# Kernel optimization log

Hardware: AMD Instinct MI355X
Metric: run time of the kernel (lower is better)

Reference implementation:

```python
import jax, jax.numpy as jnp
import numpy as np
from jax.ops import segment_sum

N = 100000
E = 1600000
IN_DIM = 128
HID_DIM = 128
OUT_DIM = 64
BN_EPS = 1e-5


def setup_inputs() -> dict:
    key = jax.random.key(0)
    ks = jax.random.split(key, 8)
    h = jax.random.normal(ks[0], (N, IN_DIM), dtype=jnp.float32)
    src = jax.random.randint(ks[1], (E,), 0, N, dtype=jnp.int32)
    dst = jax.random.randint(ks[2], (E,), 0, N, dtype=jnp.int32)
    # GraphConv weights (glorot-ish scale)
    W1 = jax.random.normal(ks[3], (IN_DIM, HID_DIM), dtype=jnp.float32) / np.sqrt(IN_DIM)
    b1 = jnp.zeros((HID_DIM,), dtype=jnp.float32)
    W2 = jax.random.normal(ks[4], (HID_DIM, OUT_DIM), dtype=jnp.float32) / np.sqrt(HID_DIM)
    b2 = jnp.zeros((OUT_DIM,), dtype=jnp.float32)
    gamma = jnp.ones((HID_DIM,), dtype=jnp.float32)
    beta = jnp.zeros((HID_DIM,), dtype=jnp.float32)
    return {"h": h, "W1": W1, "b1": b1, "W2": W2, "b2": b2,
            "gamma": gamma, "beta": beta, "src": src, "dst": dst}


def _graph_conv(h, W, b, src, dst):
    # DGL GraphConv, norm='both':
    # out = D_dst^{-1/2} * A^T (D_src^{-1/2} * h) W + b, degrees clamped to >=1
    ones = jnp.ones((E,), dtype=h.dtype)
    deg_out = jnp.clip(segment_sum(ones, src, num_segments=N), 1.0)  # out-degree of src
    deg_in = jnp.clip(segment_sum(ones, dst, num_segments=N), 1.0)   # in-degree of dst
    h = h * jax.lax.rsqrt(deg_out)[:, None]
    # apply weight before aggregation when it reduces/keeps dim (DGL optimization)
    if W.shape[0] >= W.shape[1]:
        h = h @ W
        agg = segment_sum(h[src], dst, num_segments=N)  # [N, out_feat]
    else:
        agg = segment_sum(h[src], dst, num_segments=N) @ W
    return agg * jax.lax.rsqrt(deg_in)[:, None] + b


def reference(h, W1, b1, W2, b2, gamma, beta, src, dst):
    h = _graph_conv(h, W1, b1, src, dst)           # [N, HID_DIM]
    # BatchNorm1d, training mode: batch stats over node axis, biased variance
    mean = jnp.mean(h, axis=0)
    var = jnp.mean((h - mean) ** 2, axis=0)
    h = (h - mean) * jax.lax.rsqrt(var + BN_EPS) * gamma + beta
    h = jax.nn.relu(h)
    # dropout p=0.0 -> identity
    h = _graph_conv(h, W2, b2, src, dst)           # [N, OUT_DIM]
    return h
```

## Files before the change

kernel.cpp:

```cpp
#include <hip/hip_runtime.h>

#define NN 100000
#define NE 1600000
#define NB 391
#define CAP 5120
#define EPB 8192
#define NG1 6250
#define NBN 64
#define BN_EPS 1e-5f

typedef _Float16 f16;
typedef _Float16 f16x4 __attribute__((ext_vector_type(4)));
typedef _Float16 f16x8 __attribute__((ext_vector_type(8)));
typedef float f32x4v __attribute__((ext_vector_type(4)));

__global__ __launch_bounds__(256) void kInit(const float* __restrict__ W1,
                                             const float* __restrict__ W2,
                                             f16* __restrict__ W1t,
                                             f16* __restrict__ W2t,
                                             int* __restrict__ curD,
                                             int* __restrict__ curS,
                                             float* __restrict__ stats,
                                             int* __restrict__ done) {
    int idx = blockIdx.x * 256 + threadIdx.x;
    if (idx < NB) { curD[idx] = idx * CAP; curS[idx] = idx * CAP; }
    if (idx < 512) stats[idx] = 0.f;
    if (idx == 512) done[0] = 0;
    if (idx < 16384) {
        int n = idx >> 7, k = idx & 127;
        W1t[idx] = (f16)W1[k * 128 + n];
    } else if (idx < 24576) {
        int j = idx - 16384;
        int n = j >> 7, k = j & 127;
        W2t[j] = (f16)W2[k * 64 + n];
    }
}

__global__ __launch_bounds__(512) void kC(const int* __restrict__ src,
                                          const int* __restrict__ dst,
                                          int* __restrict__ curD,
                                          int* __restrict__ curS,
                                          unsigned* __restrict__ pairs,
                                          unsigned char* __restrict__ srcBuck) {
    __shared__ int sA[EPB], dA[EPB];
    __shared__ int hD[NB], hS[NB], bD_[NB], bS_[NB];
    int t = threadIdx.x;
    for (int i = t; i < NB; i += 512) { hD[i] = 0; hS[i] = 0; }
    __syncthreads();
    int e0 = blockIdx.x * EPB;
    int ne = min(EPB, NE - e0);
    for (int i = t; i < ne; i += 512) {
        int s = src[e0 + i], d = dst[e0 + i];
        sA[i] = s; dA[i] = d;
        atomicAdd(&hD[d >> 8], 1);
        atomicAdd(&hS[s >> 8], 1);
    }
    __syncthreads();
    for (int i = t; i < NB; i += 512) {
        bD_[i] = hD[i] ? atomicAdd(&curD[i], hD[i]) : 0;
        bS_[i] = hS[i] ? atomicAdd(&curS[i], hS[i]) : 0;
        hD[i] = 0; hS[i] = 0;
    }
    __syncthreads();
    for (int i = t; i < ne; i += 512) {
        int s = sA[i], d = dA[i];
        int db = d >> 8, sb = s >> 8;
        int rD = atomicAdd(&hD[db], 1);
        int posD = bD_[db] + rD;
        int limD = (db + 1) * CAP - 1;
        if (posD > limD) posD = limD;
        pairs[posD] = ((unsigned)s << 8) | (unsigned)(d & 255);
        int rS = atomicAdd(&hS[sb], 1);
        int posS = bS_[sb] + rS;
        int limS = (sb + 1) * CAP - 1;
        if (posS > limS) posS = limS;
        srcBuck[posS] = (unsigned char)(s & 255);
    }
}

__global__ __launch_bounds__(256) void kDE(const unsigned* __restrict__ pairs,
                                           const unsigned char* __restrict__ srcBuck,
                                           const int* __restrict__ curD,
                                           const int* __restrict__ curS,
                                           int* __restrict__ rowS,
                                           int* __restrict__ rowE,
                                           int* __restrict__ col,
                                           int* __restrict__ degO) {
    __shared__ unsigned bufA[CAP];
    __shared__ int cnt[256], csc[256];
    int t = threadIdx.x;
    if (blockIdx.x < NB) {
        int b = blockIdx.x;
        int p0 = b * CAP;
        int n = min(curD[b] - p0, CAP);
        cnt[t] = 0;
        __syncthreads();
        for (int i = t; i < n; i += 256) {
            unsigned v = pairs[p0 + i];
            bufA[i] = v;
            atomicAdd(&cnt[v & 255u], 1);
        }
        __syncthreads();
        int vN = cnt[t];
        csc[t] = vN;
        __syncthreads();
        for (int off = 1; off < 256; off <<= 1) {
            int x = (t >= off) ? csc[t - off] : 0;
            __syncthreads();
            csc[t] += x;
            __syncthreads();
        }
        int nodeStart = csc[t] - vN;
        int node = b * 256 + t;
        if (node < NN) { rowS[node] = p0 + nodeStart; rowE[node] = p0 + nodeStart + vN; }
        cnt[t] = nodeStart;
        __syncthreads();
        for (int i = t; i < n; i += 256) {
            unsigned v = bufA[i];
            int r = atomicAdd(&cnt[v & 255u], 1);
            col[p0 + r] = (int)(v >> 8);
        }
    } else {
        int b = blockIdx.x - NB;
        cnt[t] = 0;
        __syncthreads();
        int p0 = b * CAP;
        int p1 = min(curS[b], p0 + CAP);
        for (int p = p0 + t; p < p1; p += 256)
            atomicAdd(&cnt[srcBuck[p]], 1);
        __syncthreads();
        int node = b * 256 + t;
        if (node < NN) degO[node] = cnt[t];
    }
}

__global__ __launch_bounds__(256) void k_gemm1(const float* __restrict__ h,
                                               const f16* __restrict__ W1t,
                                               const int* __restrict__ degO,
                                               f16* __restrict__ x1h) {
    __shared__ f16 Ah[128 * 128];
    __shared__ f16 Bt[128 * 128];
    __shared__ float rsA[128];
    int tid = threadIdx.x;
    int row0 = blockIdx.x * 128;
    if (tid < 128) {
        int r = row0 + tid;
        float d = (r < NN) ? (float)degO[r] : 1.f;
        rsA[tid] = rsqrtf(fmaxf(d, 1.f));
    }
#pragma unroll
    for (int p = 0; p < 8; ++p) {
        int fi = p * 256 + tid;
        int r = fi >> 4, c = fi & 15;
        uint4 v = *(const uint4*)&W1t[fi * 8];
        *(uint4*)&Bt[r * 128 + ((c ^ (r & 7)) * 8)] = v;
    }
    __syncthreads();
#pragma unroll
    for (int p = 0; p < 16; ++p) {
        int fi = p * 256 + tid;
        int r = fi >> 5, c4 = fi & 31;
        int grow = row0 + r;
        float4 av = float4{0.f, 0.f, 0.f, 0.f};
        if (grow < NN) av = *(const float4*)&h[(size_t)grow * 128 + c4 * 4];
        float rs = rsA[r];
        f16x4 t;
        t[0] = (f16)(av.x * rs); t[1] = (f16)(av.y * rs);
        t[2] = (f16)(av.z * rs); t[3] = (f16)(av.w * rs);
        int c8 = c4 >> 1, off = (c4 & 1) * 4;
        *(f16x4*)&Ah[r * 128 + ((c8 ^ (r & 7)) * 8) + off] = t;
    }
    __syncthreads();
    int l = tid & 63, w = tid >> 6;
    int lr = l & 15, g = l >> 4;
    int m0 = w * 32;
    f16x8 a[2][4];
#pragma unroll
    for (int m = 0; m < 2; ++m)
#pragma unroll
        for (int kk = 0; kk < 4; ++kk) {
            int row = m0 + m * 16 + lr;
            a[m][kk] = *(f16x8*)&Ah[row * 128 + (((kk * 4 + g) ^ (row & 7)) * 8)];
        }
    f32x4v acc[2][8];
#pragma unroll
    for (int m = 0; m < 2; ++m)
#pragma unroll
        for (int n = 0; n < 8; ++n) acc[m][n] = f32x4v{0.f, 0.f, 0.f, 0.f};
#pragma unroll
    for (int n = 0; n < 8; ++n) {
        int colr = n * 16 + lr;
        f16x8 b[4];
#pragma unroll
        for (int kk = 0; kk < 4; ++kk)
            b[kk] = *(f16x8*)&Bt[colr * 128 + (((kk * 4 + g) ^ (colr & 7)) * 8)];
#pragma unroll
        for (int m = 0; m < 2; ++m)
#pragma unroll
            for (int kk = 0; kk < 4; ++kk)
                acc[m][n] = __builtin_amdgcn_mfma_f32_16x16x32_f16(a[m][kk], b[kk], acc[m][n], 0, 0, 0);
    }
    __syncthreads();
#pragma unroll
    for (int m = 0; m < 2; ++m)
#pragma unroll
        for (int n = 0; n < 8; ++n)
#pragma unroll
            for (int q = 0; q < 4; ++q) {
                int row = m0 + m * 16 + g * 4 + q;
                Ah[row * 128 + n * 16 + lr] = (f16)acc[m][n][q];
            }
    __syncthreads();
#pragma unroll
    for (int p = 0; p < 8; ++p) {
        int idx = p * 64 + l;
        int r = idx >> 4, c = idx & 15;
        int row = m0 + r, grow = row0 + row;
        uint4 v = *(uint4*)&Ah[row * 128 + c * 8];
        if (grow < NN) *(uint4*)&x1h[(size_t)grow * 128 + c * 8] = v;
    }
}

__global__ __launch_bounds__(256) void k_gather1(const f16* __restrict__ x1h,
                                                 const int* __restrict__ rowS,
                                                 const int* __restrict__ rowE,
                                                 const int* __restrict__ col,
                                                 const float* __restrict__ b1,
                                                 f16* __restrict__ y1h,
                                                 float* __restrict__ part) {
    __shared__ float red[4 * 16 * 16];
    int tid = threadIdx.x;
    int bid = blockIdx.x;
    int node = bid * 16 + (tid >> 4);
    int f8 = tid & 15;
    int s0 = rowS[node], s1 = rowE[node];
    const uint4* x4 = (const uint4*)x1h;
    float acc[8] = {0.f, 0.f, 0.f, 0.f, 0.f, 0.f, 0.f, 0.f};
    int j = s0;
    for (; j + 3 < s1; j += 4) {
        int a0 = col[j], a1 = col[j + 1], a2 = col[j + 2], a3 = col[j + 3];
        uint4 v0 = x4[(size_t)a0 * 16 + f8];
        uint4 v1 = x4[(size_t)a1 * 16 + f8];
        uint4 v2 = x4[(size_t)a2 * 16 + f8];
        uint4 v3 = x4[(size_t)a3 * 16 + f8];
        const f16* h0 = (const f16*)&v0; const f16* h1 = (const f16*)&v1;
        const f16* h2 = (const f16*)&v2; const f16* h3 = (const f16*)&v3;
#pragma unroll
        for (int k = 0; k < 8; ++k)
            acc[k] += (float)h0[k] + (float)h1[k] + (float)h2[k] + (float)h3[k];
    }
    for (; j < s1; ++j) {
        int a = col[j];
        uint4 v = x4[(size_t)a * 16 + f8];
        const f16* hp = (const f16*)&v;
#pragma unroll
        for (int k = 0; k < 8; ++k) acc[k] += (float)hp[k];
    }
    float rs = rsqrtf(fmaxf((float)(s1 - s0), 1.f));
    const float4* b4 = (const float4*)b1;
    float4 ba = b4[f8 * 2], bb = b4[f8 * 2 + 1];
    f16x8 o;
    o[0] = (f16)(acc[0] * rs + ba.x); o[1] = (f16)(acc[1] * rs + ba.y);
    o[2] = (f16)(acc[2] * rs + ba.z); o[3] = (f16)(acc[3] * rs + ba.w);
    o[4] = (f16)(acc[4] * rs + bb.x); o[5] = (f16)(acc[5] * rs + bb.y);
    o[6] = (f16)(acc[6] * rs + bb.z); o[7] = (f16)(acc[7] * rs + bb.w);
    *(f16x8*)&y1h[(size_t)node * 128 + f8 * 8] = o;
    float sv[8], qv[8];
#pragma unroll
    for (int k = 0; k < 8; ++k) { sv[k] = (float)o[k]; qv[k] = sv[k] * sv[k]; }
#pragma unroll
    for (int mask = 16; mask <= 32; mask <<= 1) {
#pragma unroll
        for (int k = 0; k < 8; ++k) {
            sv[k] += __shfl_xor(sv[k], mask);
            qv[k] += __shfl_xor(qv[k], mask);
        }
    }
    int w = tid >> 6, lane = tid & 63;
    if (lane < 16) {
#pragma unroll
        for (int k = 0; k < 8; ++k) {
            red[w * 256 + lane * 16 + k] = sv[k];
            red[w * 256 + lane * 16 + 8 + k] = qv[k];
        }
    }
    __syncthreads();
    int f8_ = tid & 15, idx = tid >> 4;
    float tot = red[0 * 256 + f8_ * 16 + idx] + red[1 * 256 + f8_ * 16 + idx]
              + red[2 * 256 + f8_ * 16 + idx] + red[3 * 256 + f8_ * 16 + idx];
    int slot = (idx < 8) ? (f8_ * 8 + idx) : (128 + f8_ * 8 + (idx - 8));
    part[(size_t)bid * 256 + slot] = tot;
}

__global__ __launch_bounds__(256) void k_bnfin(const float* __restrict__ part,
                                               float* __restrict__ stats,
                                               int* __restrict__ done,
                                               const float* __restrict__ gamma,
                                               const float* __restrict__ beta) {
    int t = threadIdx.x;
    float loc = 0.f;
    for (int b = blockIdx.x; b < NG1; b += gridDim.x)
        loc += part[(size_t)b * 256 + t];
    atomicAdd(&stats[t], loc);
    __threadfence();
    __shared__ int amLast;
    if (t == 0) amLast = (atomicAdd(done, 1) == NBN - 1) ? 1 : 0;
    __syncthreads();
    if (amLast && t < 128) {
        float s  = __hip_atomic_load(&stats[t], __ATOMIC_RELAXED, __HIP_MEMORY_SCOPE_AGENT);
        float sq = __hip_atomic_load(&stats[128 + t], __ATOMIC_RELAXED, __HIP_MEMORY_SCOPE_AGENT);
        float mean = s * (1.f / NN);
        float var = sq * (1.f / NN) - mean * mean;
        var = fmaxf(var, 0.f);
        float sc = gamma[t] * rsqrtf(var + BN_EPS);
        stats[256 + t] = sc;
        stats[384 + t] = beta[t] - mean * sc;
    }
}

__global__ __launch_bounds__(256) void k_gemm2(const f16* __restrict__ y1h,
                                               const f16* __restrict__ W2t,
                                               const int* __restrict__ degO,
                                               const float* __restrict__ stats,
                                               f16* __restrict__ x2h) {
    __shared__ f16 Ah[128 * 128];
    __shared__ f16 Bt[64 * 128];
    __shared__ float sc[128], sh[128], rsA[128];
    int tid = threadIdx.x;
    int row0 = blockIdx.x * 128;
    if (tid < 128) {
        sc[tid] = stats[256 + tid];
        sh[tid] = stats[384 + tid];
        int r = row0 + tid;
        float d = (r < NN) ? (float)degO[r] : 1.f;
        rsA[tid] = rsqrtf(fmaxf(d, 1.f));
    }
#pragma unroll
    for (int p = 0; p < 4; ++p) {
        int fi = p * 256 + tid;
        int r = fi >> 4, c = fi & 15;
        uint4 v = *(const uint4*)&W2t[fi * 8];
        *(uint4*)&Bt[r * 128 + ((c ^ (r & 7)) * 8)] = v;
    }
    __syncthreads();
#pragma unroll
    for (int p = 0; p < 8; ++p) {
        int fi = p * 256 + tid;
        int r = fi >> 4, c = fi & 15;
        int grow = row0 + r;
        f16x8 t;
        if (grow < NN) {
            uint4 v = *(const uint4*)&y1h[(size_t)grow * 128 + c * 8];
            const f16* hp = (const f16*)&v;
            float rs = rsA[r];
#pragma unroll
            for (int i = 0; i < 8; ++i) {
                int ch = c * 8 + i;
                float x = (float)hp[i] * sc[ch] + sh[ch];
                t[i] = (f16)(fmaxf(x, 0.f) * rs);
            }
        } else {
#pragma unroll
            for (int i = 0; i < 8; ++i) t[i] = (f16)0.f;
        }
        *(f16x8*)&Ah[r * 128 + ((c ^ (r & 7)) * 8)] = t;
    }
    __syncthreads();
    int l = tid & 63, w = tid >> 6;
    int lr = l & 15, g = l >> 4;
    int m0 = w * 32;
    f16x8 a[2][4];
#pragma unroll
    for (int m = 0; m < 2; ++m)
#pragma unroll
        for (int kk = 0; kk < 4; ++kk) {
            int row = m0 + m * 16 + lr;
            a[m][kk] = *(f16x8*)&Ah[row * 128 + (((kk * 4 + g) ^ (row & 7)) * 8)];
        }
    f32x4v acc[2][4];
#pragma unroll
    for (int m = 0; m < 2; ++m)
#pragma unroll
        for (int n = 0; n < 4; ++n) acc[m][n] = f32x4v{0.f, 0.f, 0.f, 0.f};
#pragma unroll
    for (int n = 0; n < 4; ++n) {
        int colr = n * 16 + lr;
        f16x8 b[4];
#pragma unroll
        for (int kk = 0; kk < 4; ++kk)
            b[kk] = *(f16x8*)&Bt[colr * 128 + (((kk * 4 + g) ^ (colr & 7)) * 8)];
#pragma unroll
        for (int m = 0; m < 2; ++m)
#pragma unroll
            for (int kk = 0; kk < 4; ++kk)
                acc[m][n] = __builtin_amdgcn_mfma_f32_16x16x32_f16(a[m][kk], b[kk], acc[m][n], 0, 0, 0);
    }
    __syncthreads();
#pragma unroll
    for (int m = 0; m < 2; ++m)
#pragma unroll
        for (int n = 0; n < 4; ++n)
#pragma unroll
            for (int q = 0; q < 4; ++q) {
                int row = m0 + m * 16 + g * 4 + q;
                Ah[row * 64 + n * 16 + lr] = (f16)acc[m][n][q];
            }
    __syncthreads();
#pragma unroll
    for (int p = 0; p < 4; ++p) {
        int idx = p * 64 + l;
        int r = idx >> 3, c = idx & 7;
        int row = m0 + r, grow = row0 + row;
        uint4 v = *(uint4*)&Ah[row * 64 + c * 8];
        if (grow < NN) *(uint4*)&x2h[(size_t)grow * 64 + c * 8] = v;
    }
}

__global__ __launch_bounds__(256) void k_gather2(const f16* __restrict__ x2h,
                                                 const int* __restrict__ rowS,
                                                 const int* __restrict__ rowE,
                                                 const int* __restrict__ col,
                                                 const float* __restrict__ b2,
                                                 float* __restrict__ out) {
    int node = blockIdx.x * 32 + (threadIdx.x >> 3);
    int f8 = threadIdx.x & 7;
    if (node >= NN) return;
    int s0 = rowS[node], s1 = rowE[node];
    const uint4* x4 = (const uint4*)x2h;
    float acc[8] = {0.f, 0.f, 0.f, 0.f, 0.f, 0.f, 0.f, 0.f};
    int j = s0;
    for (; j + 3 < s1; j += 4) {
        uint4 v[4];
#pragma unroll
        for (int u = 0; u < 4; ++u)
            v[u] = x4[(size_t)col[j + u] * 8 + f8];
#pragma unroll
        for (int u = 0; u < 4; ++u) {
            const f16* hp = (const f16*)&v[u];
#pragma unroll
            for (int k = 0; k < 8; ++k) acc[k] += (float)hp[k];
        }
    }
    for (; j < s1; ++j) {
        uint4 v = x4[(size_t)col[j] * 8 + f8];
        const f16* hp = (const f16*)&v;
#pragma unroll
        for (int k = 0; k < 8; ++k) acc[k] += (float)hp[k];
    }
    float rs = rsqrtf(fmaxf((float)(s1 - s0), 1.f));
    const float4* b4 = (const float4*)b2;
    float4 ba = b4[f8 * 2], bb = b4[f8 * 2 + 1];
    float4 o0, o1;
    o0.x = acc[0] * rs + ba.x; o0.y = acc[1] * rs + ba.y;
    o0.z = acc[2] * rs + ba.z; o0.w = acc[3] * rs + ba.w;
    o1.x = acc[4] * rs + bb.x; o1.y = acc[5] * rs + bb.y;
    o1.z = acc[6] * rs + bb.z; o1.w = acc[7] * rs + bb.w;
    *(float4*)&out[(size_t)node * 64 + f8 * 8] = o0;
    *(float4*)&out[(size_t)node * 64 + f8 * 8 + 4] = o1;
}

extern "C" void kernel_launch(void* const* d_in, const int* in_sizes, int n_in,
                              void* d_out, int out_size, void* d_ws, size_t ws_size,
                              hipStream_t stream) {
    const float* h     = (const float*)d_in[0];
    const float* W1    = (const float*)d_in[1];
    const float* b1    = (const float*)d_in[2];
    const float* W2    = (const float*)d_in[3];
    const float* b2    = (const float*)d_in[4];
    const float* gamma = (const float*)d_in[5];
    const float* beta  = (const float*)d_in[6];
    const int*   src   = (const int*)d_in[7];
    const int*   dst   = (const int*)d_in[8];
    float* out = (float*)d_out;

    const size_t BSZ = (size_t)NB * CAP;

    int* base = (int*)d_ws;
    float* stats = (float*)base;
    int* done = base + 512;
    int* curD = base + 513;
    int* curS = curD + NB;
    int* rowS = curS + NB;
    int* rowE = rowS + NN;
    int* degO = rowE + NN;
    int* col  = degO + NN;
    unsigned* pairs = (unsigned*)(col + BSZ);
    unsigned char* srcBuck = (unsigned char*)(pairs + BSZ);
    float* part = (float*)(pairs + BSZ + (BSZ + 3) / 4);
    size_t o = (size_t)(col + BSZ - base) + BSZ + (BSZ + 3) / 4 + (size_t)NG1 * 256;
    o = (o + 3) & ~(size_t)3;
    f16* W1t = (f16*)(base + o);
    f16* W2t = W1t + 16384;
    o += 8192 + 4096;
    f16* x1h = (f16*)(base + o);
    o += (size_t)NN * 64;
    f16* y1h = (f16*)(base + o);
    f16* x2h = x1h;

    kInit<<<97, 256, 0, stream>>>(W1, W2, W1t, W2t, curD, curS, stats, done);

    int bgrid = (NE + EPB - 1) / EPB;
    kC<<<bgrid, 512, 0, stream>>>(src, dst, curD, curS, pairs, srcBuck);
    kDE<<<2 * NB, 256, 0, stream>>>(pairs, srcBuck, curD, curS, rowS, rowE, col, degO);

    int ggrid = (NN + 127) / 128;
    k_gemm1<<<ggrid, 256, 0, stream>>>(h, W1t, degO, x1h);
    k_gather1<<<NG1, 256, 0, stream>>>(x1h, rowS, rowE, col, b1, y1h, part);
    k_bnfin<<<NBN, 256, 0, stream>>>(part, stats, done, gamma, beta);
    k_gemm2<<<ggrid, 256, 0, stream>>>(y1h, W2t, degO, stats, x2h);
    k_gather2<<<(NN + 31) / 32, 256, 0, stream>>>(x2h, rowS, rowE, col, b2, out);
}
```

Measured before the change: 252.6 us.

## Fuse GEMM1 with CSR build, move out-degree scaling into gathers

Out-degree normalization now happens inside the gather kernels: each neighbor's row is scaled by a per-node rsqrt(out-degree) read per edge. GEMM1 no longer depends on degrees, so it runs in the same launch as the CSR build and degree count, with blocks split by index and shared memory held in a union. The init kernel is replaced by a memset, the weight transpose is merged into the bucketing kernel, and bucket counters become relative offsets. This cuts launches and lets GEMM1 overlap the sort, at the cost of an extra scattered per-edge load of rsO in both gathers.

```diff
diff --git a/kernel.cpp b/kernel.cpp
--- a/kernel.cpp
+++ b/kernel.cpp
@@ -5,6 +5,7 @@
 #define NB 391
 #define CAP 5120
 #define EPB 8192
+#define G1B 782
 #define NG1 6250
 #define NBN 64
 #define BN_EPS 1e-5f
@@ -14,37 +15,28 @@
 typedef _Float16 f16x8 __attribute__((ext_vector_type(8)));
 typedef float f32x4v __attribute__((ext_vector_type(4)));
 
-__global__ __launch_bounds__(256) void kInit(const float* __restrict__ W1,
-                                             const float* __restrict__ W2,
-                                             f16* __restrict__ W1t,
-                                             f16* __restrict__ W2t,
-                                             int* __restrict__ curD,
-                                             int* __restrict__ curS,
-                                             float* __restrict__ stats,
-                                             int* __restrict__ done) {
-    int idx = blockIdx.x * 256 + threadIdx.x;
-    if (idx < NB) { curD[idx] = idx * CAP; curS[idx] = idx * CAP; }
-    if (idx < 512) stats[idx] = 0.f;
-    if (idx == 512) done[0] = 0;
-    if (idx < 16384) {
-        int n = idx >> 7, k = idx & 127;
-        W1t[idx] = (f16)W1[k * 128 + n];
-    } else if (idx < 24576) {
-        int j = idx - 16384;
+__global__ __launch_bounds__(512) void kCW(const int* __restrict__ src,
+                                           const int* __restrict__ dst,
+                                           const float* __restrict__ W1,
+                                           const float* __restrict__ W2,
+                                           f16* __restrict__ W1t,
+                                           f16* __restrict__ W2t,
+                                           int* __restrict__ curD,
+                                           int* __restrict__ curS,
+                                           unsigned* __restrict__ pairs,
+                                           unsigned char* __restrict__ srcBuck) {
+    int t = threadIdx.x;
+    int gidx = blockIdx.x * 512 + t;
+    if (gidx < 16384) {
+        int n = gidx >> 7, k = gidx & 127;
+        W1t[gidx] = (f16)W1[k * 128 + n];
+    } else if (gidx < 24576) {
+        int j = gidx - 16384;
         int n = j >> 7, k = j & 127;
         W2t[j] = (f16)W2[k * 64 + n];
     }
-}
-
-__global__ __launch_bounds__(512) void kC(const int* __restrict__ src,
-                                          const int* __restrict__ dst,
-                                          int* __restrict__ curD,
-                                          int* __restrict__ curS,
-                                          unsigned* __restrict__ pairs,
-                                          unsigned char* __restrict__ srcBuck) {
     __shared__ int sA[EPB], dA[EPB];
     __shared__ int hD[NB], hS[NB], bD_[NB], bS_[NB];
-    int t = threadIdx.x;
     for (int i = t; i < NB; i += 512) { hD[i] = 0; hS[i] = 0; }
     __syncthreads();
     int e0 = blockIdx.x * EPB;
@@ -66,33 +58,115 @@
         int s = sA[i], d = dA[i];
         int db = d >> 8, sb = s >> 8;
         int rD = atomicAdd(&hD[db], 1);
-        int posD = bD_[db] + rD;
-        int limD = (db + 1) * CAP - 1;
-        if (posD > limD) posD = limD;
-        pairs[posD] = ((unsigned)s << 8) | (unsigned)(d & 255);
+        int offD = bD_[db] + rD;
+        if (offD > CAP - 1) offD = CAP - 1;
+        pairs[db * CAP + offD] = ((unsigned)s << 8) | (unsigned)(d & 255);
         int rS = atomicAdd(&hS[sb], 1);
-        int posS = bS_[sb] + rS;
-        int limS = (sb + 1) * CAP - 1;
-        if (posS > limS) posS = limS;
-        srcBuck[posS] = (unsigned char)(s & 255);
-    }
-}
-
-__global__ __launch_bounds__(256) void kDE(const unsigned* __restrict__ pairs,
+        int offS = bS_[sb] + rS;
+        if (offS > CAP - 1) offS = CAP - 1;
+        srcBuck[sb * CAP + offS] = (unsigned char)(s & 255);
+    }
+}
+
+union SMem {
+    struct { f16 Ah[128 * 128]; f16 Bt[128 * 128]; } g;
+    struct { unsigned bufA[CAP]; int cnt[256]; int csc[256]; } c;
+    struct { int cnt[256]; } d;
+};
+
+__global__ __launch_bounds__(256) void kDG(const float* __restrict__ h,
+                                           const f16* __restrict__ W1t,
+                                           const unsigned* __restrict__ pairs,
                                            const unsigned char* __restrict__ srcBuck,
                                            const int* __restrict__ curD,
                                            const int* __restrict__ curS,
                                            int* __restrict__ rowS,
                                            int* __restrict__ rowE,
                                            int* __restrict__ col,
-                                           int* __restrict__ degO) {
-    __shared__ unsigned bufA[CAP];
-    __shared__ int cnt[256], csc[256];
+                                           float* __restrict__ rsO,
+                                           f16* __restrict__ x1h) {
+    __shared__ SMem sm;
     int t = threadIdx.x;
-    if (blockIdx.x < NB) {
-        int b = blockIdx.x;
+    if (blockIdx.x < G1B) {
+        f16* Ah = sm.g.Ah;
+        f16* Bt = sm.g.Bt;
+        int row0 = blockIdx.x * 128;
+#pragma unroll
+        for (int p = 0; p < 8; ++p) {
+            int fi = p * 256 + t;
+            int r = fi >> 4, c = fi & 15;
+            uint4 v = *(const uint4*)&W1t[fi * 8];
+            *(uint4*)&Bt[r * 128 + ((c ^ (r & 7)) * 8)] = v;
+        }
+#pragma unroll
+        for (int p = 0; p < 16; ++p) {
+            int fi = p * 256 + t;
+            int r = fi >> 5, c4 = fi & 31;
+            int grow = row0 + r;
+            float4 av = float4{0.f, 0.f, 0.f, 0.f};
+            if (grow < NN) av = *(const float4*)&h[(size_t)grow * 128 + c4 * 4];
+            f16x4 tt;
+            tt[0] = (f16)av.x; tt[1] = (f16)av.y;
+            tt[2] = (f16)av.z; tt[3] = (f16)av.w;
+            int c8 = c4 >> 1, off = (c4 & 1) * 4;
+            *(f16x4*)&Ah[r * 128 + ((c8 ^ (r & 7)) * 8) + off] = tt;
+        }
+        __syncthreads();
+        int l = t & 63, w = t >> 6;
+        int lr = l & 15, g = l >> 4;
+        int m0 = w * 32;
+        f16x8 a[2][4];
+#pragma unroll
+        for (int m = 0; m < 2; ++m)
+#pragma unroll
+            for (int kk = 0; kk < 4; ++kk) {
+                int row = m0 + m * 16 + lr;
+                a[m][kk] = *(f16x8*)&Ah[row * 128 + (((kk * 4 + g) ^ (row & 7)) * 8)];
+            }
+        f32x4v acc[2][8];
+#pragma unroll
+        for (int m = 0; m < 2; ++m)
+#pragma unroll
+            for (int n = 0; n < 8; ++n) acc[m][n] = f32x4v{0.f, 0.f, 0.f, 0.f};
+#pragma unroll
+        for (int n = 0; n < 8; ++n) {
+            int colr = n * 16 + lr;
+            f16x8 b[4];
+#pragma unroll
+            for (int kk = 0; kk < 4; ++kk)
+                b[kk] = *(f16x8*)&Bt[colr * 128 + (((kk * 4 + g) ^ (colr & 7)) * 8)];
+#pragma unroll
+            for (int m = 0; m < 2; ++m)
+#pragma unroll
+                for (int kk = 0; kk < 4; ++kk)
+                    acc[m][n] = __builtin_amdgcn_mfma_f32_16x16x32_f16(a[m][kk], b[kk], acc[m][n], 0, 0, 0);
+        }
+        __syncthreads();
+#pragma unroll
+        for (int m = 0; m < 2; ++m)
+#pragma unroll
+            for (int n = 0; n < 8; ++n)
+#pragma unroll
+                for (int q = 0; q < 4; ++q) {
+                    int row = m0 + m * 16 + g * 4 + q;
+                    Ah[row * 128 + n * 16 + lr] = (f16)acc[m][n][q];
+                }
+        __syncthreads();
+#pragma unroll
+        for (int p = 0; p < 8; ++p) {
+            int idx = p * 64 + l;
+            int r = idx >> 4, c = idx & 15;
+            int row = m0 + r, grow = row0 + row;
+            uint4 v = *(uint4*)&Ah[row * 128 + c * 8];
+            if (grow < NN) *(uint4*)&x1h[(size_t)grow * 128 + c * 8] = v;
+        }
+    } else if (blockIdx.x < G1B + NB) {
+        int b = blockIdx.x - G1B;
+        unsigned* bufA = sm.c.bufA;
+        int* cnt = sm.c.cnt;
+        int* csc = sm.c.csc;
         int p0 = b * CAP;
-        int n = min(curD[b] - p0, CAP);
+        int n = min(curD[b], CAP);
         cnt[t] = 0;
         __syncthreads();
         for (int i = t; i < n; i += 256) {
@@ -121,103 +195,17 @@
             col[p0 + r] = (int)(v >> 8);
         }
     } else {
-        int b = blockIdx.x - NB;
+        int b = blockIdx.x - G1B - NB;
+        int* cnt = sm.d.cnt;
         cnt[t] = 0;
         __syncthreads();
         int p0 = b * CAP;
-        int p1 = min(curS[b], p0 + CAP);
-        for (int p = p0 + t; p < p1; p += 256)
-            atomicAdd(&cnt[srcBuck[p]], 1);
+        int n = min(curS[b], CAP);
+        for (int p = t; p < n; p += 256)
+            atomicAdd(&cnt[srcBuck[p0 + p]], 1);
         __syncthreads();
         int node = b * 256 + t;
-        if (node < NN) degO[node] = cnt[t];
-    }
-}
-
-__global__ __launch_bounds__(256) void k_gemm1(const float* __restrict__ h,
-                                               const f16* __restrict__ W1t,
-                                               const int* __restrict__ degO,
-                                               f16* __restrict__ x1h) {
-    __shared__ f16 Ah[128 * 128];
-    __shared__ f16 Bt[128 * 128];
-    __shared__ float rsA[128];
-    int tid = threadIdx.x;
-    int row0 = blockIdx.x * 128;
-    if (tid < 128) {
-        int r = row0 + tid;
-        float d = (r < NN) ? (float)degO[r] : 1.f;
-        rsA[tid] = rsqrtf(fmaxf(d, 1.f));
-    }
-#pragma unroll
-    for (int p = 0; p < 8; ++p) {
-        int fi = p * 256 + tid;
-        int r = fi >> 4, c = fi & 15;
-        uint4 v = *(const uint4*)&W1t[fi * 8];
-        *(uint4*)&Bt[r * 128 + ((c ^ (r & 7)) * 8)] = v;
-    }
-    __syncthreads();
-#pragma unroll
-    for (int p = 0; p < 16; ++p) {
-        int fi = p * 256 + tid;
-        int r = fi >> 5, c4 = fi & 31;
-        int grow = row0 + r;
-        float4 av = float4{0.f, 0.f, 0.f, 0.f};
-        if (grow < NN) av = *(const float4*)&h[(size_t)grow * 128 + c4 * 4];
-        float rs = rsA[r];
-        f16x4 t;
-        t[0] = (f16)(av.x * rs); t[1] = (f16)(av.y * rs);
-        t[2] = (f16)(av.z * rs); t[3] = (f16)(av.w * rs);
-        int c8 = c4 >> 1, off = (c4 & 1) * 4;
-        *(f16x4*)&Ah[r * 128 + ((c8 ^ (r & 7)) * 8) + off] = t;
-    }
-    __syncthreads();
-    int l = tid & 63, w = tid >> 6;
-    int lr = l & 15, g = l >> 4;
-    int m0 = w * 32;
-    f16x8 a[2][4];
-#pragma unroll
-    for (int m = 0; m < 2; ++m)
-#pragma unroll
-        for (int kk = 0; kk < 4; ++kk) {
-            int row = m0 + m * 16 + lr;
-            a[m][kk] = *(f16x8*)&Ah[row * 128 + (((kk * 4 + g) ^ (row & 7)) * 8)];
-        }
-    f32x4v acc[2][8];
-#pragma unroll
-    for (int m = 0; m < 2; ++m)
-#pragma unroll
-        for (int n = 0; n < 8; ++n) acc[m][n] = f32x4v{0.f, 0.f, 0.f, 0.f};
-#pragma unroll
-    for (int n = 0; n < 8; ++n) {
-        int colr = n * 16 + lr;
-        f16x8 b[4];
-#pragma unroll
-        for (int kk = 0; kk < 4; ++kk)
-            b[kk] = *(f16x8*)&Bt[colr * 128 + (((kk * 4 + g) ^ (colr & 7)) * 8)];
-#pragma unroll
-        for (int m = 0; m < 2; ++m)
-#pragma unroll
-            for (int kk = 0; kk < 4; ++kk)
-                acc[m][n] = __builtin_amdgcn_mfma_f32_16x16x32_f16(a[m][kk], b[kk], acc[m][n], 0, 0, 0);
-    }
-    __syncthreads();
-#pragma unroll
-    for (int m = 0; m < 2; ++m)
-#pragma unroll
-        for (int n = 0; n < 8; ++n)
-#pragma unroll
-            for (int q = 0; q < 4; ++q) {
-                int row = m0 + m * 16 + g * 4 + q;
-                Ah[row * 128 + n * 16 + lr] = (f16)acc[m][n][q];
-            }
-    __syncthreads();
-#pragma unroll
-    for (int p = 0; p < 8; ++p) {
-        int idx = p * 64 + l;
-        int r = idx >> 4, c = idx & 15;
-        int row = m0 + r, grow = row0 + row;
-        uint4 v = *(uint4*)&Ah[row * 128 + c * 8];
-        if (grow < NN) *(uint4*)&x1h[(size_t)grow * 128 + c * 8] = v;
+        if (node < NN) rsO[node] = rsqrtf(fmaxf((float)cnt[t], 1.f));
     }
 }
 
@@ -225,6 +213,7 @@
                                                  const int* __restrict__ rowS,
                                                  const int* __restrict__ rowE,
                                                  const int* __restrict__ col,
+                                                 const float* __restrict__ rsO,
                                                  const float* __restrict__ b1,
                                                  f16* __restrict__ y1h,
                                                  float* __restrict__ part) {
@@ -239,6 +228,7 @@
     int j = s0;
     for (; j + 3 < s1; j += 4) {
         int a0 = col[j], a1 = col[j + 1], a2 = col[j + 2], a3 = col[j + 3];
+        float r0 = rsO[a0], r1 = rsO[a1], r2 = rsO[a2], r3 = rsO[a3];
         uint4 v0 = x4[(size_t)a0 * 16 + f8];
         uint4 v1 = x4[(size_t)a1 * 16 + f8];
         uint4 v2 = x4[(size_t)a2 * 16 + f8];
@@ -247,14 +237,16 @@
         const f16* h2 = (const f16*)&v2; const f16* h3 = (const f16*)&v3;
 #pragma unroll
         for (int k = 0; k < 8; ++k)
-            acc[k] += (float)h0[k] + (float)h1[k] + (float)h2[k] + (float)h3[k];
+            acc[k] += r0 * (float)h0[k] + r1 * (float)h1[k]
+                    + r2 * (float)h2[k] + r3 * (float)h3[k];
     }
     for (; j < s1; ++j) {
         int a = col[j];
+        float r = rsO[a];
         uint4 v = x4[(size_t)a * 16 + f8];
         const f16* hp = (const f16*)&v;
 #pragma unroll
-        for (int k = 0; k < 8; ++k) acc[k] += (float)hp[k];
+        for (int k = 0; k < 8; ++k) acc[k] += r * (float)hp[k];
     }
     float rs = rsqrtf(fmaxf((float)(s1 - s0), 1.f));
     const float4* b4 = (const float4*)b1;
@@ -320,21 +312,14 @@
 
 __global__ __launch_bounds__(256) void k_gemm2(const f16* __restrict__ y1h,
                                                const f16* __restrict__ W2t,
-                                               const int* __restrict__ degO,
                                                const float* __restrict__ stats,
                                                f16* __restrict__ x2h) {
     __shared__ f16 Ah[128 * 128];
     __shared__ f16 Bt[64 * 128];
-    __shared__ float sc[128], sh[128], rsA[128];
+    __shared__ float sc[128], sh[128];
     int tid = threadIdx.x;
     int row0 = blockIdx.x * 128;
-    if (tid < 128) {
-        sc[tid] = stats[256 + tid];
-        sh[tid] = stats[384 + tid];
-        int r = row0 + tid;
-        float d = (r < NN) ? (float)degO[r] : 1.f;
-        rsA[tid] = rsqrtf(fmaxf(d, 1.f));
-    }
+    if (tid < 128) { sc[tid] = stats[256 + tid]; sh[tid] = stats[384 + tid]; }
 #pragma unroll
     for (int p = 0; p < 4; ++p) {
         int fi = p * 256 + tid;
@@ -352,12 +337,11 @@
         if (grow < NN) {
             uint4 v = *(const uint4*)&y1h[(size_t)grow * 128 + c * 8];
             const f16* hp = (const f16*)&v;
-            float rs = rsA[r];
 #pragma unroll
             for (int i = 0; i < 8; ++i) {
                 int ch = c * 8 + i;
                 float x = (float)hp[i] * sc[ch] + sh[ch];
-                t[i] = (f16)(fmaxf(x, 0.f) * rs);
+                t[i] = (f16)fmaxf(x, 0.f);
             }
         } else {
 #pragma unroll
@@ -420,6 +404,7 @@
                                                  const int* __restrict__ rowS,
                                                  const int* __restrict__ rowE,
                                                  const int* __restrict__ col,
+                                                 const float* __restrict__ rsO,
                                                  const float* __restrict__ b2,
                                                  float* __restrict__ out) {
     int node = blockIdx.x * 32 + (threadIdx.x >> 3);
@@ -430,22 +415,26 @@
     float acc[8] = {0.f, 0.f, 0.f, 0.f, 0.f, 0.f, 0.f, 0.f};
     int j = s0;
     for (; j + 3 < s1; j += 4) {
-        uint4 v[4];
-#pragma unroll
-        for (int u = 0; u < 4; ++u)
-            v[u] = x4[(size_t)col[j + u] * 8 + f8];
-#pragma unroll
-        for (int u = 0; u < 4; ++u) {
-            const f16* hp = (const f16*)&v[u];
-#pragma unroll
-            for (int k = 0; k < 8; ++k) acc[k] += (float)hp[k];
-        }
+        int a0 = col[j], a1 = col[j + 1], a2 = col[j + 2], a3 = col[j + 3];
+        float r0 = rsO[a0], r1 = rsO[a1], r2 = rsO[a2], r3 = rsO[a3];
+        uint4 v0 = x4[(size_t)a0 * 8 + f8];
+        uint4 v1 = x4[(size_t)a1 * 8 + f8];
+        uint4 v2 = x4[(size_t)a2 * 8 + f8];
+        uint4 v3 = x4[(size_t)a3 * 8 + f8];
+        const f16* h0 = (const f16*)&v0; const f16* h1 = (const f16*)&v1;
+        const f16* h2 = (const f16*)&v2; const f16* h3 = (const f16*)&v3;
+#pragma unroll
+        for (int k = 0; k < 8; ++k)
+            acc[k] += r0 * (float)h0[k] + r1 * (float)h1[k]
+                    + r2 * (float)h2[k] + r3 * (float)h3[k];
     }
     for (; j < s1; ++j) {
-        uint4 v = x4[(size_t)col[j] * 8 + f8];
+        int a = col[j];
+        float r = rsO[a];
+        uint4 v = x4[(size_t)a * 8 + f8];
         const f16* hp = (const f16*)&v;
 #pragma unroll
-        for (int k = 0; k < 8; ++k) acc[k] += (float)hp[k];
+        for (int k = 0; k < 8; ++k) acc[k] += r * (float)hp[k];
     }
     float rs = rsqrtf(fmaxf((float)(s1 - s0), 1.f));
     const float4* b4 = (const float4*)b2;
@@ -482,8 +471,8 @@
     int* curS = curD + NB;
     int* rowS = curS + NB;
     int* rowE = rowS + NN;
-    int* degO = rowE + NN;
-    int* col  = degO + NN;
+    float* rsO = (float*)(rowE + NN);
+    int* col  = (int*)(rsO + NN);
     unsigned* pairs = (unsigned*)(col + BSZ);
     unsigned char* srcBuck = (unsigned char*)(pairs + BSZ);
     float* part = (float*)(pairs + BSZ + (BSZ + 3) / 4);
@@ -497,16 +486,14 @@
     f16* y1h = (f16*)(base + o);
     f16* x2h = x1h;
 
-    kInit<<<97, 256, 0, stream>>>(W1, W2, W1t, W2t, curD, curS, stats, done);
+    hipMemsetAsync(base, 0, (size_t)(513 + 2 * NB) * 4, stream);
 
     int bgrid = (NE + EPB - 1) / EPB;
-    kC<<<bgrid, 512, 0, stream>>>(src, dst, curD, curS, pairs, srcBuck);
-    kDE<<<2 * NB, 256, 0, stream>>>(pairs, srcBuck, curD, curS, rowS, rowE, col, degO);
-
-    int ggrid = (NN + 127) / 128;
-    k_gemm1<<<ggrid, 256, 0, stream>>>(h, W1t, degO, x1h);
-    k_gather1<<<NG1, 256, 0, stream>>>(x1h, rowS, rowE, col, b1, y1h, part);
+    kCW<<<bgrid, 512, 0, stream>>>(src, dst, W1, W2, W1t, W2t, curD, curS, pairs, srcBuck);
+    kDG<<<G1B + 2 * NB, 256, 0, stream>>>(h, W1t, pairs, srcBuck, curD, curS,
+                                          rowS, rowE, col, rsO, x1h);
+    k_gather1<<<NG1, 256, 0, stream>>>(x1h, rowS, rowE, col, rsO, b1, y1h, part);
     k_bnfin<<<NBN, 256, 0, stream>>>(part, stats, done, gamma, beta);
-    k_gemm2<<<ggrid, 256, 0, stream>>>(y1h, W2t, degO, stats, x2h);
-    k_gather2<<<(NN + 31) / 32, 256, 0, stream>>>(x2h, rowS, rowE, col, b2, out);
-}
+    k_gemm2<<<(NN + 127) / 128, 256, 0, stream>>>(y1h, W2t, stats, x2h);
+    k_gather2<<<(NN + 31) / 32, 256, 0, stream>>>(x2h, rowS, rowE, col, rsO, b2, out);
+}
```

Result: slower. 257.8 us (+2.0%).
